# Kernel optimization log

Measured on AMD Instinct MI355X. Metric: run time of the kernel, lower is better.

The kernel has to match this reference:

```python
import jax, jax.numpy as jnp
import numpy as np

NUM_GROUPS = 131072
GROUP_SIZE = 3          # trigenic interaction queries (Dango)
HIDDEN = 128
NUM_HEADS = 4
HEAD_DIM = HIDDEN // NUM_HEADS
NUM_LAYERS = 2


def setup_inputs() -> dict:
    key = jax.random.key(0)
    ks = jax.random.split(key, 16)
    N = NUM_GROUPS * GROUP_SIZE
    H, L = HIDDEN, NUM_LAYERS
    s = 1.0 / np.sqrt(H)
    inp = {
        "gene_embeddings": jax.random.normal(ks[0], (N, H), dtype=jnp.float32),
        "batch": jnp.repeat(jnp.arange(NUM_GROUPS, dtype=jnp.int64), GROUP_SIZE),
        # static embedding Linear
        "Ws": jax.random.uniform(ks[1], (H, H), jnp.float32, -s, s),
        "bs": jnp.zeros((H,), jnp.float32),
        # per-layer attention projections, stacked over layers
        "Wq": jax.random.uniform(ks[2], (L, H, H), jnp.float32, -s, s),
        "bq": jnp.zeros((L, H), jnp.float32),
        "Wk": jax.random.uniform(ks[3], (L, H, H), jnp.float32, -s, s),
        "bk": jnp.zeros((L, H), jnp.float32),
        "Wv": jax.random.uniform(ks[4], (L, H, H), jnp.float32, -s, s),
        "bv": jnp.zeros((L, H), jnp.float32),
        "Wo": jax.random.uniform(ks[5], (L, H, H), jnp.float32, -s, s),
        "bo": jnp.zeros((L, H), jnp.float32),
        # ReZero params, init 0.01 as in module
        "beta": jnp.full((L,), 0.01, jnp.float32),
        # prediction layer (xavier_uniform)
        "Wp": jax.random.uniform(ks[6], (H, 1), jnp.float32, -np.sqrt(6.0 / (H + 1)), np.sqrt(6.0 / (H + 1))),
        "bp": jnp.zeros((1,), jnp.float32),
    }
    return inp


def _attention_layer(xg, Wq, bq, Wk, bk, Wv, bv, Wo, bo, beta):
    # xg: [G, S, H] block-diagonal groups; exclude-self masked MHA + ReZero.
    G, S, H = xg.shape
    q = (xg @ Wq + bq).reshape(G, S, NUM_HEADS, HEAD_DIM)
    k = (xg @ Wk + bk).reshape(G, S, NUM_HEADS, HEAD_DIM)
    v = (xg @ Wv + bv).reshape(G, S, NUM_HEADS, HEAD_DIM)
    scores = jnp.einsum("gqhd,gkhd->ghqk", q, k) / np.sqrt(HEAD_DIM)
    self_mask = jnp.eye(S, dtype=bool)  # exclude self-attention
    scores = jnp.where(self_mask, -jnp.inf, scores)
    attn = jax.nn.softmax(scores, axis=-1)
    attn = jnp.nan_to_num(attn, nan=0.0)  # torch.nan_to_num parity
    out = jnp.einsum("ghqk,gkhd->gqhd", attn, v).reshape(G, S, H)
    out = out @ Wo + bo
    return xg + beta * out  # ReZero residual (dropout: eval mode identity)


def reference(gene_embeddings, batch, Ws, bs, Wq, bq, Wk, bk, Wv, bv, Wo, bo, beta, Wp, bp):
    N, H = gene_embeddings.shape
    G = N // GROUP_SIZE
    static = jax.nn.relu(gene_embeddings @ Ws + bs)  # static embedding MLP
    dyn = gene_embeddings.reshape(G, GROUP_SIZE, H)
    for i in range(NUM_LAYERS):
        dyn = _attention_layer(dyn, Wq[i], bq[i], Wk[i], bk[i],
                               Wv[i], bv[i], Wo[i], bo[i], beta[i])
    dyn = dyn.reshape(N, H)
    diff_sq = (dyn - static) ** 2
    gene_scores = (diff_sq @ Wp + bp).squeeze(-1)  # [N]
    # scatter_mean over batch ids
    sums = jax.ops.segment_sum(gene_scores, batch, num_segments=G)
    cnts = jax.ops.segment_sum(jnp.ones_like(gene_scores), batch, num_segments=G)
    interaction_scores = sums / jnp.maximum(cnts, 1.0)
    return interaction_scores[:, None]  # [G, 1]
```

## Files before the change

### kernel.cpp

```cpp
#include <hip/hip_runtime.h>
#include <hip/hip_bf16.h>

#define NGROUPS 131072
#define H 128
#define SG 3
#define NHEADS 4
#define HD 32
#define GB 16
#define MR 48
#define NT 512
#define NLAYERS 2
#define NSLOT 7
#define BVO_OFF (NSLOT * H * H)

typedef unsigned short u16;
typedef unsigned int u32;
typedef __bf16 bf16x8 __attribute__((ext_vector_type(8)));
typedef float floatx4 __attribute__((ext_vector_type(4)));

__device__ __forceinline__ float bf2f_lo(u32 u) {
  union { u32 i; float f; } c; c.i = u << 16; return c.f;
}
__device__ __forceinline__ float bf2f_hi(u32 u) {
  union { u32 i; float f; } c; c.i = u & 0xffff0000u; return c.f;
}
__device__ __forceinline__ u32 f2bf2(float a, float b) {
  __hip_bfloat162 h = __float22bfloat162_rn(make_float2(a, b));
  union { __hip_bfloat162 h; u32 u; } c; c.h = h; return c.u;
}
__device__ __forceinline__ u16 f2bf(float f) {
  union { float f; u32 i; } c; c.f = f;
  u32 x = c.i; x += 0x7fffu + ((x >> 16) & 1u);
  return (u16)(x >> 16);
}

__device__ __forceinline__ const u16* swz(const u16* base, int row, int bcol) {
  return base + row * H + ((bcol ^ ((row & 7) << 4)) >> 1);
}
__device__ __forceinline__ u16* swz(u16* base, int row, int bcol) {
  return base + row * H + ((bcol ^ ((row & 7) << 4)) >> 1);
}

__global__ void wconv_t(const float* __restrict__ Ws, const float* __restrict__ Wq,
                        const float* __restrict__ Wk, u16* __restrict__ wt) {
  int idx = blockIdx.x * 256 + threadIdx.x;
  int s5 = idx >> 14, rem = idx & 16383;
  int n = rem >> 7, k = rem & 127;
  const float* src; int dst;
  switch (s5) {
    case 0:  src = Ws;         dst = 0; break;
    case 1:  src = Wq;         dst = 1; break;
    case 2:  src = Wk;         dst = 2; break;
    case 3:  src = Wq + H * H; dst = 4; break;
    default: src = Wk + H * H; dst = 5; break;
  }
  wt[dst * (H * H) + rem] = f2bf(src[k * H + n]);
}

__global__ void wvo_kernel(const float* __restrict__ Wv, const float* __restrict__ Wo,
                           const float* __restrict__ bv, u16* __restrict__ wt) {
  if (blockIdx.x < 128) {
    int idx = blockIdx.x * 256 + threadIdx.x;
    int l = idx >> 14, rem = idx & 16383;
    int k = rem >> 7, n = rem & 127;
    const float* wv = Wv + l * H * H + k * H;
    const float* wo = Wo + l * H * H + n;
    float s = 0.f;
#pragma unroll 8
    for (int m = 0; m < H; m++) s += wv[m] * wo[m * H];
    wt[(3 + 3 * l) * (H * H) + n * H + k] = f2bf(s);
  } else {
    int t = threadIdx.x;
    int l = t >> 7, n = t & 127;
    const float* bvl = bv + l * H;
    const float* wo = Wo + l * H * H + n;
    float s = 0.f;
#pragma unroll 8
    for (int m = 0; m < H; m++) s += bvl[m] * wo[m * H];
    reinterpret_cast<float*>(wt + BVO_OFF)[l * H + n] = s;
  }
}

template <int NP>
__device__ __forceinline__ void multi_proj(const u16* __restrict__ lds,
                                           const u16* __restrict__ w0,
                                           floatx4 acc[NP][3], int m0, int qi, int wrow) {
#pragma unroll
  for (int p = 0; p < NP; p++)
#pragma unroll
    for (int nt = 0; nt < 3; nt++)
      acc[p][nt] = (floatx4){0.f, 0.f, 0.f, 0.f};
#pragma unroll
  for (int kk = 0; kk < 4; kk++) {
    bf16x8 b[3];
#pragma unroll
    for (int nt = 0; nt < 3; nt++)
      b[nt] = *reinterpret_cast<const bf16x8*>(swz(lds, nt * 16 + m0, kk * 64 + qi * 16));
#pragma unroll
    for (int p = 0; p < NP; p++) {
      bf16x8 a = *reinterpret_cast<const bf16x8*>(w0 + (size_t)p * H * H + wrow * H + kk * 32 + qi * 8);
#pragma unroll
      for (int nt = 0; nt < 3; nt++)
        acc[p][nt] = __builtin_amdgcn_mfma_f32_16x16x32_bf16(a, b[nt], acc[p][nt], 0, 0, 0);
    }
  }
}

__device__ __forceinline__ void store_proj(u16* __restrict__ buf, const floatx4 acc[3],
                                           float4 b4, int m0, int colb) {
#pragma unroll
  for (int nt = 0; nt < 3; nt++) {
    uint2 pp;
    pp.x = f2bf2(acc[nt][0] + b4.x, acc[nt][1] + b4.y);
    pp.y = f2bf2(acc[nt][2] + b4.z, acc[nt][3] + b4.w);
    *reinterpret_cast<uint2*>(swz(buf, nt * 16 + m0, colb * 2)) = pp;
  }
}

__global__ void __launch_bounds__(NT)
__attribute__((amdgpu_waves_per_eu(4)))
dango_kernel(const float* __restrict__ x, const u16* __restrict__ wt,
             const float* __restrict__ bs, const float* __restrict__ bq,
             const float* __restrict__ bk, const float* __restrict__ bo,
             const float* __restrict__ beta, const float* __restrict__ Wp,
             const float* __restrict__ bp, float* __restrict__ out)
{
  __shared__ __align__(16) u16 qbuf[MR][H];
  __shared__ __align__(16) u16 kbuf[MR][H];
  __shared__ __align__(16) u16 vbuf[MR][H];
  __shared__ __align__(16) float scratch[GB * NHEADS * SG * 2];

  const int tid = threadIdx.x;
  const int lane = tid & 63;
  const int wave = tid >> 6;
  const int m0 = lane & 15;
  const int qi = lane >> 4;
  const int colb = wave * 16 + qi * 4;
  const int wrow = wave * 16 + m0;
  const int row0 = blockIdx.x * MR;
  const float* __restrict__ bvo = reinterpret_cast<const float*>(wt + BVO_OFF);

  float xdyn[3][4];
  u32 statpk[3][2];

#pragma unroll
  for (int nt = 0; nt < 3; nt++) {
    int row = nt * 16 + m0;
    float4 v = *reinterpret_cast<const float4*>(x + (size_t)(row0 + row) * H + colb);
    xdyn[nt][0] = v.x; xdyn[nt][1] = v.y; xdyn[nt][2] = v.z; xdyn[nt][3] = v.w;
    uint2 pp; pp.x = f2bf2(v.x, v.y); pp.y = f2bf2(v.z, v.w);
    *reinterpret_cast<uint2*>(swz(&qbuf[0][0], row, colb * 2)) = pp;
  }
  __syncthreads();

  {
    floatx4 acc[4][3];
    multi_proj<4>(&qbuf[0][0], wt, acc, m0, qi, wrow);
    {
      float4 b4 = *reinterpret_cast<const float4*>(bs + colb);
#pragma unroll
      for (int nt = 0; nt < 3; nt++) {
        statpk[nt][0] = f2bf2(fmaxf(acc[0][nt][0] + b4.x, 0.f), fmaxf(acc[0][nt][1] + b4.y, 0.f));
        statpk[nt][1] = f2bf2(fmaxf(acc[0][nt][2] + b4.z, 0.f), fmaxf(acc[0][nt][3] + b4.w, 0.f));
      }
    }
    store_proj(&kbuf[0][0], acc[2], *reinterpret_cast<const float4*>(bk + colb), m0, colb);
    store_proj(&vbuf[0][0], acc[3], *reinterpret_cast<const float4*>(bvo + colb), m0, colb);
    __syncthreads();
    store_proj(&qbuf[0][0], acc[1], *reinterpret_cast<const float4*>(bq + colb), m0, colb);
  }
  __syncthreads();

  for (int l = 0; l < NLAYERS; l++) {
    if (tid < GB * NHEADS * SG) {
      int g = tid / (NHEADS * SG);
      int rem = tid % (NHEADS * SG);
      int h = rem / SG;
      int i = rem % SG;
      int j0 = (i == 0) ? 1 : 0;
      int j1 = (i == 2) ? 1 : 2;
      float s0 = 0.f, s1 = 0.f;
#pragma unroll
      for (int c = 0; c < 4; c++) {
        int bcol = h * (HD * 2) + c * 16;
        uint4 qu = *reinterpret_cast<const uint4*>(swz(&qbuf[0][0], g * 3 + i,  bcol));
        uint4 u0 = *reinterpret_cast<const uint4*>(swz(&kbuf[0][0], g * 3 + j0, bcol));
        uint4 u1 = *reinterpret_cast<const uint4*>(swz(&kbuf[0][0], g * 3 + j1, bcol));
        u32 qs[4] = {qu.x, qu.y, qu.z, qu.w};
        u32 a0[4] = {u0.x, u0.y, u0.z, u0.w};
        u32 a1[4] = {u1.x, u1.y, u1.z, u1.w};
#pragma unroll
        for (int e = 0; e < 4; e++) {
          float ql = bf2f_lo(qs[e]), qh = bf2f_hi(qs[e]);
          s0 += ql * bf2f_lo(a0[e]) + qh * bf2f_hi(a0[e]);
          s1 += ql * bf2f_lo(a1[e]) + qh * bf2f_hi(a1[e]);
        }
      }
      s0 *= 0.17677669529663687f;
      s1 *= 0.17677669529663687f;
      float mx = fmaxf(s0, s1);
      float e0 = __expf(s0 - mx), e1 = __expf(s1 - mx);
      float inv = 1.f / (e0 + e1);
      int ai = ((g * NHEADS + h) * SG + i) * 2;
      scratch[ai + 0] = e0 * inv;
      scratch[ai + 1] = e1 * inv;
    }
    __syncthreads();

    {
      float4 bo4 = *reinterpret_cast<const float4*>(bo + l * H + colb);
      const float betal = beta[l];
      const int h = colb >> 5;
#pragma unroll
      for (int nt = 0; nt < 3; nt++) {
        int r = nt * 16 + m0;
        int g = r / 3, i = r - g * 3;
        int j0 = (i == 0) ? 1 : 0;
        int j1 = (i == 2) ? 1 : 2;
        int ai = ((g * NHEADS + h) * SG + i) * 2;
        float a0 = scratch[ai + 0], a1 = scratch[ai + 1];
        uint2 v0 = *reinterpret_cast<const uint2*>(swz(&vbuf[0][0], g * 3 + j0, colb * 2));
        uint2 v1 = *reinterpret_cast<const uint2*>(swz(&vbuf[0][0], g * 3 + j1, colb * 2));
        xdyn[nt][0] += betal * (a0 * bf2f_lo(v0.x) + a1 * bf2f_lo(v1.x) + bo4.x);
        xdyn[nt][1] += betal * (a0 * bf2f_hi(v0.x) + a1 * bf2f_hi(v1.x) + bo4.y);
        xdyn[nt][2] += betal * (a0 * bf2f_lo(v0.y) + a1 * bf2f_lo(v1.y) + bo4.z);
        xdyn[nt][3] += betal * (a0 * bf2f_hi(v0.y) + a1 * bf2f_hi(v1.y) + bo4.w);
        if (l + 1 < NLAYERS) {
          uint2 pp;
          pp.x = f2bf2(xdyn[nt][0], xdyn[nt][1]);
          pp.y = f2bf2(xdyn[nt][2], xdyn[nt][3]);
          *reinterpret_cast<uint2*>(swz(&qbuf[0][0], r, colb * 2)) = pp;
        }
      }
    }
    __syncthreads();

    if (l + 1 < NLAYERS) {
      floatx4 acc[3][3];
      multi_proj<3>(&qbuf[0][0], wt + (size_t)(1 + 3 * (l + 1)) * H * H, acc, m0, qi, wrow);
      store_proj(&kbuf[0][0], acc[1], *reinterpret_cast<const float4*>(bk + (l + 1) * H + colb), m0, colb);
      store_proj(&vbuf[0][0], acc[2], *reinterpret_cast<const float4*>(bvo + (l + 1) * H + colb), m0, colb);
      __syncthreads();
      store_proj(&qbuf[0][0], acc[0], *reinterpret_cast<const float4*>(bq + (l + 1) * H + colb), m0, colb);
      __syncthreads();
    }
  }

  float4 wp4 = *reinterpret_cast<const float4*>(Wp + colb);
  float rsum[3];
#pragma unroll
  for (int nt = 0; nt < 3; nt++) {
    float d0 = xdyn[nt][0] - bf2f_lo(statpk[nt][0]);
    float d1 = xdyn[nt][1] - bf2f_hi(statpk[nt][0]);
    float d2 = xdyn[nt][2] - bf2f_lo(statpk[nt][1]);
    float d3 = xdyn[nt][3] - bf2f_hi(statpk[nt][1]);
    rsum[nt] = d0 * d0 * wp4.x + d1 * d1 * wp4.y + d2 * d2 * wp4.z + d3 * d3 * wp4.w;
  }
#pragma unroll
  for (int nt = 0; nt < 3; nt++) {
    rsum[nt] += __shfl_xor(rsum[nt], 16, 64);
    rsum[nt] += __shfl_xor(rsum[nt], 32, 64);
  }
  if (qi == 0) {
#pragma unroll
    for (int nt = 0; nt < 3; nt++)
      scratch[(nt * 16 + m0) * 8 + wave] = rsum[nt];
  }
  __syncthreads();
  if (tid < GB) {
    float s = 0.f;
#pragma unroll
    for (int i = 0; i < SG; i++) {
      int row = tid * 3 + i;
#pragma unroll
      for (int w = 0; w < 8; w++) s += scratch[row * 8 + w];
    }
    out[blockIdx.x * GB + tid] = s * (1.f / 3.f) + bp[0];
  }
}

extern "C" void kernel_launch(void* const* d_in, const int* in_sizes, int n_in,
                              void* d_out, int out_size, void* d_ws, size_t ws_size,
                              hipStream_t stream) {
  const float* x    = (const float*)d_in[0];
  const float* Ws   = (const float*)d_in[2];
  const float* bs   = (const float*)d_in[3];
  const float* Wq   = (const float*)d_in[4];
  const float* bq   = (const float*)d_in[5];
  const float* Wk   = (const float*)d_in[6];
  const float* bk   = (const float*)d_in[7];
  const float* Wv   = (const float*)d_in[8];
  const float* bv   = (const float*)d_in[9];
  const float* Wo   = (const float*)d_in[10];
  const float* bo   = (const float*)d_in[11];
  const float* beta = (const float*)d_in[12];
  const float* Wp   = (const float*)d_in[13];
  const float* bp   = (const float*)d_in[14];
  float* out = (float*)d_out;
  u16* wt = (u16*)d_ws;

  wconv_t<<<320, 256, 0, stream>>>(Ws, Wq, Wk, wt);
  wvo_kernel<<<129, 256, 0, stream>>>(Wv, Wo, bv, wt);
  dango_kernel<<<NGROUPS / GB, NT, 0, stream>>>(x, wt, bs, bq, bk, bo, beta, Wp, bp, out);
}
```

Before: 581.1 us.

## Split projection GEMMs into smaller batches and parallelize score computation per key

```diff
diff --git a/kernel.cpp b/kernel.cpp
--- a/kernel.cpp
+++ b/kernel.cpp
@@ -117,6 +117,22 @@
   }
 }
 
+__device__ __forceinline__ void pack_proj(u32 pk[3][2], const floatx4 acc[3], float4 b4) {
+#pragma unroll
+  for (int nt = 0; nt < 3; nt++) {
+    pk[nt][0] = f2bf2(acc[nt][0] + b4.x, acc[nt][1] + b4.y);
+    pk[nt][1] = f2bf2(acc[nt][2] + b4.z, acc[nt][3] + b4.w);
+  }
+}
+__device__ __forceinline__ void store_packed(u16* __restrict__ buf, const u32 pk[3][2],
+                                             int m0, int colb) {
+#pragma unroll
+  for (int nt = 0; nt < 3; nt++) {
+    uint2 pp; pp.x = pk[nt][0]; pp.y = pk[nt][1];
+    *reinterpret_cast<uint2*>(swz(buf, nt * 16 + m0, colb * 2)) = pp;
+  }
+}
+
 __global__ void __launch_bounds__(NT)
 __attribute__((amdgpu_waves_per_eu(4)))
 dango_kernel(const float* __restrict__ x, const u16* __restrict__ wt,
@@ -142,6 +158,7 @@
 
   float xdyn[3][4];
   u32 statpk[3][2];
+  u32 qpk[3][2];
 
 #pragma unroll
   for (int nt = 0; nt < 3; nt++) {
@@ -154,8 +171,8 @@
   __syncthreads();
 
   {
-    floatx4 acc[4][3];
-    multi_proj<4>(&qbuf[0][0], wt, acc, m0, qi, wrow);
+    floatx4 acc[2][3];
+    multi_proj<2>(&qbuf[0][0], wt, acc, m0, qi, wrow);
     {
       float4 b4 = *reinterpret_cast<const float4*>(bs + colb);
 #pragma unroll
@@ -164,46 +181,43 @@
         statpk[nt][1] = f2bf2(fmaxf(acc[0][nt][2] + b4.z, 0.f), fmaxf(acc[0][nt][3] + b4.w, 0.f));
       }
     }
-    store_proj(&kbuf[0][0], acc[2], *reinterpret_cast<const float4*>(bk + colb), m0, colb);
-    store_proj(&vbuf[0][0], acc[3], *reinterpret_cast<const float4*>(bvo + colb), m0, colb);
-    __syncthreads();
-    store_proj(&qbuf[0][0], acc[1], *reinterpret_cast<const float4*>(bq + colb), m0, colb);
+    pack_proj(qpk, acc[1], *reinterpret_cast<const float4*>(bq + colb));
+  }
+  {
+    floatx4 acc[2][3];
+    multi_proj<2>(&qbuf[0][0], wt + (size_t)2 * H * H, acc, m0, qi, wrow);
+    store_proj(&kbuf[0][0], acc[0], *reinterpret_cast<const float4*>(bk + colb), m0, colb);
+    store_proj(&vbuf[0][0], acc[1], *reinterpret_cast<const float4*>(bvo + colb), m0, colb);
   }
   __syncthreads();
+  store_packed(&qbuf[0][0], qpk, m0, colb);
+  __syncthreads();
 
   for (int l = 0; l < NLAYERS; l++) {
-    if (tid < GB * NHEADS * SG) {
-      int g = tid / (NHEADS * SG);
-      int rem = tid % (NHEADS * SG);
-      int h = rem / SG;
-      int i = rem % SG;
-      int j0 = (i == 0) ? 1 : 0;
-      int j1 = (i == 2) ? 1 : 2;
-      float s0 = 0.f, s1 = 0.f;
+    if (tid < GB * NHEADS * SG * 2) {
+      int js = tid & 1;
+      int rest = tid >> 1;
+      int i = rest % 3;
+      int m = rest / 3;
+      int h = m & 3, g = m >> 2;
+      int j = (i == 0) ? (js ? 2 : 1) : (i == 1) ? (js ? 2 : 0) : (js ? 1 : 0);
+      float s = 0.f;
 #pragma unroll
       for (int c = 0; c < 4; c++) {
-        int bcol = h * (HD * 2) + c * 16;
-        uint4 qu = *reinterpret_cast<const uint4*>(swz(&qbuf[0][0], g * 3 + i,  bcol));
-        uint4 u0 = *reinterpret_cast<const uint4*>(swz(&kbuf[0][0], g * 3 + j0, bcol));
-        uint4 u1 = *reinterpret_cast<const uint4*>(swz(&kbuf[0][0], g * 3 + j1, bcol));
+        int bcol = h * 64 + c * 16;
+        uint4 qu = *reinterpret_cast<const uint4*>(swz(&qbuf[0][0], g * 3 + i, bcol));
+        uint4 ku = *reinterpret_cast<const uint4*>(swz(&kbuf[0][0], g * 3 + j, bcol));
         u32 qs[4] = {qu.x, qu.y, qu.z, qu.w};
-        u32 a0[4] = {u0.x, u0.y, u0.z, u0.w};
-        u32 a1[4] = {u1.x, u1.y, u1.z, u1.w};
-#pragma unroll
-        for (int e = 0; e < 4; e++) {
-          float ql = bf2f_lo(qs[e]), qh = bf2f_hi(qs[e]);
-          s0 += ql * bf2f_lo(a0[e]) + qh * bf2f_hi(a0[e]);
-          s1 += ql * bf2f_lo(a1[e]) + qh * bf2f_hi(a1[e]);
-        }
-      }
-      s0 *= 0.17677669529663687f;
-      s1 *= 0.17677669529663687f;
-      float mx = fmaxf(s0, s1);
-      float e0 = __expf(s0 - mx), e1 = __expf(s1 - mx);
-      float inv = 1.f / (e0 + e1);
-      int ai = ((g * NHEADS + h) * SG + i) * 2;
-      scratch[ai + 0] = e0 * inv;
-      scratch[ai + 1] = e1 * inv;
+        u32 ks[4] = {ku.x, ku.y, ku.z, ku.w};
+#pragma unroll
+        for (int e = 0; e < 4; e++)
+          s += bf2f_lo(qs[e]) * bf2f_lo(ks[e]) + bf2f_hi(qs[e]) * bf2f_hi(ks[e]);
+      }
+      s *= 0.17677669529663687f;
+      float so = __shfl_xor(s, 1);
+      float mx = fmaxf(s, so);
+      float e = __expf(s - mx), eo = __expf(so - mx);
+      scratch[((g * NHEADS + h) * SG + i) * 2 + js] = e / (e + eo);
     }
     __syncthreads();
 
@@ -236,12 +250,20 @@
     __syncthreads();
 
     if (l + 1 < NLAYERS) {
-      floatx4 acc[3][3];
-      multi_proj<3>(&qbuf[0][0], wt + (size_t)(1 + 3 * (l + 1)) * H * H, acc, m0, qi, wrow);
-      store_proj(&kbuf[0][0], acc[1], *reinterpret_cast<const float4*>(bk + (l + 1) * H + colb), m0, colb);
-      store_proj(&vbuf[0][0], acc[2], *reinterpret_cast<const float4*>(bvo + (l + 1) * H + colb), m0, colb);
+      const size_t base = (size_t)(1 + 3 * (l + 1));
+      {
+        floatx4 acc[2][3];
+        multi_proj<2>(&qbuf[0][0], wt + base * H * H, acc, m0, qi, wrow);
+        pack_proj(qpk, acc[0], *reinterpret_cast<const float4*>(bq + (l + 1) * H + colb));
+        store_proj(&kbuf[0][0], acc[1], *reinterpret_cast<const float4*>(bk + (l + 1) * H + colb), m0, colb);
+      }
+      {
+        floatx4 acc1[1][3];
+        multi_proj<1>(&qbuf[0][0], wt + (base + 2) * H * H, acc1, m0, qi, wrow);
+        store_proj(&vbuf[0][0], acc1[0], *reinterpret_cast<const float4*>(bvo + (l + 1) * H + colb), m0, colb);
+      }
       __syncthreads();
-      store_proj(&qbuf[0][0], acc[0], *reinterpret_cast<const float4*>(bq + (l + 1) * H + colb), m0, colb);
+      store_packed(&qbuf[0][0], qpk, m0, colb);
       __syncthreads();
     }
   }
```

After: 647.2 us. 1.11x slower.

## Use padded LDS rows and separate input buffer; split attention scores across threads

Applied to the files above, without the earlier changes.

```diff
diff --git a/kernel.cpp b/kernel.cpp
--- a/kernel.cpp
+++ b/kernel.cpp
@@ -9,6 +9,7 @@
 #define GB 16
 #define MR 48
 #define NT 512
+#define BP 136
 #define NLAYERS 2
 #define NSLOT 7
 #define BVO_OFF (NSLOT * H * H)
@@ -32,13 +33,6 @@
   union { float f; u32 i; } c; c.f = f;
   u32 x = c.i; x += 0x7fffu + ((x >> 16) & 1u);
   return (u16)(x >> 16);
-}
-
-__device__ __forceinline__ const u16* swz(const u16* base, int row, int bcol) {
-  return base + row * H + ((bcol ^ ((row & 7) << 4)) >> 1);
-}
-__device__ __forceinline__ u16* swz(u16* base, int row, int bcol) {
-  return base + row * H + ((bcol ^ ((row & 7) << 4)) >> 1);
 }
 
 __global__ void wconv_t(const float* __restrict__ Ws, const float* __restrict__ Wq,
@@ -95,7 +89,7 @@
     bf16x8 b[3];
 #pragma unroll
     for (int nt = 0; nt < 3; nt++)
-      b[nt] = *reinterpret_cast<const bf16x8*>(swz(lds, nt * 16 + m0, kk * 64 + qi * 16));
+      b[nt] = *reinterpret_cast<const bf16x8*>(lds + (nt * 16 + m0) * BP + kk * 32 + qi * 8);
 #pragma unroll
     for (int p = 0; p < NP; p++) {
       bf16x8 a = *reinterpret_cast<const bf16x8*>(w0 + (size_t)p * H * H + wrow * H + kk * 32 + qi * 8);
@@ -113,7 +107,7 @@
     uint2 pp;
     pp.x = f2bf2(acc[nt][0] + b4.x, acc[nt][1] + b4.y);
     pp.y = f2bf2(acc[nt][2] + b4.z, acc[nt][3] + b4.w);
-    *reinterpret_cast<uint2*>(swz(buf, nt * 16 + m0, colb * 2)) = pp;
+    *reinterpret_cast<uint2*>(buf + (nt * 16 + m0) * BP + colb) = pp;
   }
 }
 
@@ -125,9 +119,10 @@
              const float* __restrict__ beta, const float* __restrict__ Wp,
              const float* __restrict__ bp, float* __restrict__ out)
 {
-  __shared__ __align__(16) u16 qbuf[MR][H];
-  __shared__ __align__(16) u16 kbuf[MR][H];
-  __shared__ __align__(16) u16 vbuf[MR][H];
+  __shared__ __align__(16) u16 xbf[MR][BP];
+  __shared__ __align__(16) u16 qbuf[MR][BP];
+  __shared__ __align__(16) u16 kbuf[MR][BP];
+  __shared__ __align__(16) u16 vbuf[MR][BP];
   __shared__ __align__(16) float scratch[GB * NHEADS * SG * 2];
 
   const int tid = threadIdx.x;
@@ -149,13 +144,13 @@
     float4 v = *reinterpret_cast<const float4*>(x + (size_t)(row0 + row) * H + colb);
     xdyn[nt][0] = v.x; xdyn[nt][1] = v.y; xdyn[nt][2] = v.z; xdyn[nt][3] = v.w;
     uint2 pp; pp.x = f2bf2(v.x, v.y); pp.y = f2bf2(v.z, v.w);
-    *reinterpret_cast<uint2*>(swz(&qbuf[0][0], row, colb * 2)) = pp;
+    *reinterpret_cast<uint2*>(&xbf[row][colb]) = pp;
   }
   __syncthreads();
 
   {
     floatx4 acc[4][3];
-    multi_proj<4>(&qbuf[0][0], wt, acc, m0, qi, wrow);
+    multi_proj<4>(&xbf[0][0], wt, acc, m0, qi, wrow);
     {
       float4 b4 = *reinterpret_cast<const float4*>(bs + colb);
 #pragma unroll
@@ -164,46 +159,37 @@
         statpk[nt][1] = f2bf2(fmaxf(acc[0][nt][2] + b4.z, 0.f), fmaxf(acc[0][nt][3] + b4.w, 0.f));
       }
     }
+    store_proj(&qbuf[0][0], acc[1], *reinterpret_cast<const float4*>(bq + colb), m0, colb);
     store_proj(&kbuf[0][0], acc[2], *reinterpret_cast<const float4*>(bk + colb), m0, colb);
     store_proj(&vbuf[0][0], acc[3], *reinterpret_cast<const float4*>(bvo + colb), m0, colb);
-    __syncthreads();
-    store_proj(&qbuf[0][0], acc[1], *reinterpret_cast<const float4*>(bq + colb), m0, colb);
   }
   __syncthreads();
 
   for (int l = 0; l < NLAYERS; l++) {
-    if (tid < GB * NHEADS * SG) {
-      int g = tid / (NHEADS * SG);
-      int rem = tid % (NHEADS * SG);
-      int h = rem / SG;
-      int i = rem % SG;
-      int j0 = (i == 0) ? 1 : 0;
-      int j1 = (i == 2) ? 1 : 2;
-      float s0 = 0.f, s1 = 0.f;
+    if (tid < GB * NHEADS * SG * 2) {
+      int js = tid & 1;
+      int rest = tid >> 1;
+      int i = rest % 3;
+      int m = rest / 3;
+      int h = m & 3, g = m >> 2;
+      int j = (i == 0) ? (js ? 2 : 1) : (i == 1) ? (js ? 2 : 0) : (js ? 1 : 0);
+      const uint4* qp = reinterpret_cast<const uint4*>(&qbuf[g * 3 + i][h * HD]);
+      const uint4* kp = reinterpret_cast<const uint4*>(&kbuf[g * 3 + j][h * HD]);
+      float s = 0.f;
 #pragma unroll
       for (int c = 0; c < 4; c++) {
-        int bcol = h * (HD * 2) + c * 16;
-        uint4 qu = *reinterpret_cast<const uint4*>(swz(&qbuf[0][0], g * 3 + i,  bcol));
-        uint4 u0 = *reinterpret_cast<const uint4*>(swz(&kbuf[0][0], g * 3 + j0, bcol));
-        uint4 u1 = *reinterpret_cast<const uint4*>(swz(&kbuf[0][0], g * 3 + j1, bcol));
+        uint4 qu = qp[c], ku = kp[c];
         u32 qs[4] = {qu.x, qu.y, qu.z, qu.w};
-        u32 a0[4] = {u0.x, u0.y, u0.z, u0.w};
-        u32 a1[4] = {u1.x, u1.y, u1.z, u1.w};
-#pragma unroll
-        for (int e = 0; e < 4; e++) {
-          float ql = bf2f_lo(qs[e]), qh = bf2f_hi(qs[e]);
-          s0 += ql * bf2f_lo(a0[e]) + qh * bf2f_hi(a0[e]);
-          s1 += ql * bf2f_lo(a1[e]) + qh * bf2f_hi(a1[e]);
-        }
+        u32 ks[4] = {ku.x, ku.y, ku.z, ku.w};
+#pragma unroll
+        for (int e = 0; e < 4; e++)
+          s += bf2f_lo(qs[e]) * bf2f_lo(ks[e]) + bf2f_hi(qs[e]) * bf2f_hi(ks[e]);
       }
-      s0 *= 0.17677669529663687f;
-      s1 *= 0.17677669529663687f;
-      float mx = fmaxf(s0, s1);
-      float e0 = __expf(s0 - mx), e1 = __expf(s1 - mx);
-      float inv = 1.f / (e0 + e1);
-      int ai = ((g * NHEADS + h) * SG + i) * 2;
-      scratch[ai + 0] = e0 * inv;
-      scratch[ai + 1] = e1 * inv;
+      s *= 0.17677669529663687f;
+      float so = __shfl_xor(s, 1);
+      float mx = fmaxf(s, so);
+      float e = __expf(s - mx), eo = __expf(so - mx);
+      scratch[((g * NHEADS + h) * SG + i) * 2 + js] = e / (e + eo);
     }
     __syncthreads();
 
@@ -219,8 +205,8 @@
         int j1 = (i == 2) ? 1 : 2;
         int ai = ((g * NHEADS + h) * SG + i) * 2;
         float a0 = scratch[ai + 0], a1 = scratch[ai + 1];
-        uint2 v0 = *reinterpret_cast<const uint2*>(swz(&vbuf[0][0], g * 3 + j0, colb * 2));
-        uint2 v1 = *reinterpret_cast<const uint2*>(swz(&vbuf[0][0], g * 3 + j1, colb * 2));
+        uint2 v0 = *reinterpret_cast<const uint2*>(&vbuf[g * 3 + j0][colb]);
+        uint2 v1 = *reinterpret_cast<const uint2*>(&vbuf[g * 3 + j1][colb]);
         xdyn[nt][0] += betal * (a0 * bf2f_lo(v0.x) + a1 * bf2f_lo(v1.x) + bo4.x);
         xdyn[nt][1] += betal * (a0 * bf2f_hi(v0.x) + a1 * bf2f_hi(v1.x) + bo4.y);
         xdyn[nt][2] += betal * (a0 * bf2f_lo(v0.y) + a1 * bf2f_lo(v1.y) + bo4.z);
@@ -229,7 +215,7 @@
           uint2 pp;
           pp.x = f2bf2(xdyn[nt][0], xdyn[nt][1]);
           pp.y = f2bf2(xdyn[nt][2], xdyn[nt][3]);
-          *reinterpret_cast<uint2*>(swz(&qbuf[0][0], r, colb * 2)) = pp;
+          *reinterpret_cast<uint2*>(&xbf[r][colb]) = pp;
         }
       }
     }
@@ -237,11 +223,10 @@
 
     if (l + 1 < NLAYERS) {
       floatx4 acc[3][3];
-      multi_proj<3>(&qbuf[0][0], wt + (size_t)(1 + 3 * (l + 1)) * H * H, acc, m0, qi, wrow);
+      multi_proj<3>(&xbf[0][0], wt + (size_t)(1 + 3 * (l + 1)) * H * H, acc, m0, qi, wrow);
+      store_proj(&qbuf[0][0], acc[0], *reinterpret_cast<const float4*>(bq + (l + 1) * H + colb), m0, colb);
       store_proj(&kbuf[0][0], acc[1], *reinterpret_cast<const float4*>(bk + (l + 1) * H + colb), m0, colb);
       store_proj(&vbuf[0][0], acc[2], *reinterpret_cast<const float4*>(bvo + (l + 1) * H + colb), m0, colb);
-      __syncthreads();
-      store_proj(&qbuf[0][0], acc[0], *reinterpret_cast<const float4*>(bq + (l + 1) * H + colb), m0, colb);
       __syncthreads();
     }
   }
```

Measured after the change: 531.6 us. 8.5% less time.
